# Performance work log

Hardware: AMD Instinct MI355X
Metric: run time of the kernel (lower is better)

## Reference

```python
import jax, jax.numpy as jnp
import numpy as np

BN_EPS = 1e-5  # torch BatchNorm1d default


def setup_inputs() -> dict:
    key = jax.random.key(0)
    k = jax.random.split(key, 5)
    B, D, L = 4096, 4096, 4  # batch, width, num layers (3 hidden + 1 output)
    x = jax.random.normal(k[0], (B, D), dtype=jnp.float32)
    # Per-layer Linear weights stored as [L, in, out]; scaled like xavier-ish init.
    W = jax.random.normal(k[1], (L, D, D), dtype=jnp.float32) * (1.0 / np.sqrt(D))
    b = jax.random.normal(k[2], (L, D), dtype=jnp.float32) * 0.01
    gamma = jax.random.uniform(k[3], (L, D), dtype=jnp.float32, minval=0.5, maxval=1.5)
    beta = jax.random.normal(k[4], (L, D), dtype=jnp.float32) * 0.1
    return {"x": x, "W": W, "b": b, "gamma": gamma, "beta": beta}


def _layer(h, W_l, b_l, gamma_l, beta_l):
    # one big GEMM replaces the per-neuron GEMV loop + stack
    h = h @ W_l + b_l  # [B, out]
    # BatchNorm1d, training mode: biased batch stats over the batch dim
    mu = jnp.mean(h, axis=0)
    var = jnp.var(h, axis=0)
    h = (h - mu) * jax.lax.rsqrt(var + BN_EPS) * gamma_l + beta_l
    return jax.nn.relu(h)


def reference(x, W, b, gamma, beta):
    out = x
    for l in range(W.shape[0]):  # small fixed layer count
        out = _layer(out, W[l], b[l], gamma[l], beta[l])
    # nn.Softmax(dim=0): softmax over the batch dimension, as in the original
    return jax.nn.softmax(out, axis=0)
```

## Files before the change

### kernel.cpp

```cpp
#include <hip/hip_runtime.h>
#include <stdint.h>

#define DIMD 4096
#define DIMB 4096
#define NLAYER 4
#define NT (DIMD / 64)

typedef unsigned short u16;
typedef __attribute__((ext_vector_type(4))) float f32x4;
typedef __attribute__((ext_vector_type(8))) __bf16 bf16x8;

__device__ __forceinline__ u16 f2bf(float f) {
    union { float f; uint32_t u; } v; v.f = f;
    return (u16)((v.u + 0x7fffu + ((v.u >> 16) & 1u)) >> 16);
}

__global__ void k_cvt(const float* __restrict__ in, u16* __restrict__ out) {
    int i = (blockIdx.x * 256 + threadIdx.x) * 4;
    float4 v = *reinterpret_cast<const float4*>(in + i);
    ushort4 r;
    r.x = f2bf(v.x); r.y = f2bf(v.y); r.z = f2bf(v.z); r.w = f2bf(v.w);
    *reinterpret_cast<ushort4*>(out + i) = r;
}

__global__ void k_trans(const float* __restrict__ W, u16* __restrict__ Wt) {
    __shared__ float tile[64][65];
    const int t = threadIdx.x;
    const int n0 = blockIdx.x * 64, k0 = blockIdx.y * 64;
    const int kr = t >> 4, c4 = (t & 15) * 4;
    #pragma unroll
    for (int r = 0; r < 4; ++r) {
        float4 v = *reinterpret_cast<const float4*>(W + (size_t)(k0 + kr + r * 16) * DIMD + n0 + c4);
        tile[kr + r * 16][c4 + 0] = v.x;
        tile[kr + r * 16][c4 + 1] = v.y;
        tile[kr + r * 16][c4 + 2] = v.z;
        tile[kr + r * 16][c4 + 3] = v.w;
    }
    __syncthreads();
    const int nr = t >> 4, k4 = (t & 15) * 4;
    #pragma unroll
    for (int r = 0; r < 4; ++r) {
        int n = nr + r * 16;
        ushort4 o;
        o.x = f2bf(tile[k4 + 0][n]);
        o.y = f2bf(tile[k4 + 1][n]);
        o.z = f2bf(tile[k4 + 2][n]);
        o.w = f2bf(tile[k4 + 3][n]);
        *reinterpret_cast<ushort4*>(Wt + (size_t)(n0 + n) * DIMD + k0 + k4) = o;
    }
}

#define GLD(g, l) __builtin_amdgcn_global_load_lds( \
    (__attribute__((address_space(1))) void*)(g),   \
    (__attribute__((address_space(3))) void*)(l), 16, 0, 0)

__global__ __launch_bounds__(512, 2) void k_gemm(
        const u16* __restrict__ A, const u16* __restrict__ Bt,
        const float* __restrict__ bias, float* __restrict__ C,
        float* __restrict__ csum, float* __restrict__ csum2) {
    __shared__ __attribute__((aligned(16))) u16 As[2 * 256 * 64];
    __shared__ __attribute__((aligned(16))) u16 Bs[2 * 256 * 64];
    const int tid = threadIdx.x;
    const int lane = tid & 63, wv = tid >> 6;
    const int wm = wv >> 2, wn = wv & 3;
    const int bm = blockIdx.y, bn = blockIdx.x;
    const int lr = lane & 15, lk = lane >> 4;

    const int r0 = tid >> 3;
    const int cswz = (tid & 7) ^ (r0 & 7);
    const u16* gA = A  + (size_t)(bm * 256 + r0) * DIMD + cswz * 8;
    const u16* gB = Bt + (size_t)(bn * 256 + r0) * DIMD + cswz * 8;

#define STAGE_A(h, t, buf) do { \
    const u16* _s = gA + (size_t)(h) * 128 * DIMD + (size_t)(t) * 64; \
    u16* _d = As + (buf) * 16384 + (h) * 8192 + wv * 512; \
    GLD(_s, _d); GLD(_s + (size_t)64 * DIMD, _d + 4096); \
} while (0)
#define STAGE_B(h, t, buf) do { \
    const u16* _s = gB + (size_t)(h) * 128 * DIMD + (size_t)(t) * 64; \
    u16* _d = Bs + (buf) * 16384 + (h) * 8192 + wv * 512; \
    GLD(_s, _d); GLD(_s + (size_t)64 * DIMD, _d + 4096); \
} while (0)

    int aoff[4][2], boff[2][2];
    #pragma unroll
    for (int mf = 0; mf < 4; ++mf)
        #pragma unroll
        for (int ks = 0; ks < 2; ++ks) {
            int row = wm * 128 + mf * 16 + lr;
            aoff[mf][ks] = row * 64 + ((ks * 4 + lk) ^ (row & 7)) * 8;
        }
    #pragma unroll
    for (int nf = 0; nf < 2; ++nf)
        #pragma unroll
        for (int ks = 0; ks < 2; ++ks) {
            int row = wn * 64 + nf * 16 + lr;
            boff[nf][ks] = row * 64 + ((ks * 4 + lk) ^ (row & 7)) * 8;
        }

    f32x4 acc[8][4] = {};
    bf16x8 a[4][2], b0[2][2], b1[2][2];

    STAGE_B(0, 0, 0); STAGE_B(1, 0, 0); STAGE_A(0, 0, 0); STAGE_A(1, 0, 0);
    STAGE_B(0, 1, 1); STAGE_B(1, 1, 1); STAGE_A(0, 1, 1); STAGE_A(1, 1, 1);
    asm volatile("s_waitcnt vmcnt(8)" ::: "memory");
    __builtin_amdgcn_s_barrier();

    for (int t = 0; t < NT; ++t) {
        const int cur = t & 1;
        const u16* Ab = As + cur * 16384;
        const u16* Bb = Bs + cur * 16384;
        const bool pf = (t + 2 < NT);

        #pragma unroll
        for (int mf = 0; mf < 4; ++mf)
            #pragma unroll
            for (int ks = 0; ks < 2; ++ks)
                a[mf][ks] = *reinterpret_cast<const bf16x8*>(Ab + aoff[mf][ks]);
        #pragma unroll
        for (int nf = 0; nf < 2; ++nf)
            #pragma unroll
            for (int ks = 0; ks < 2; ++ks)
                b0[nf][ks] = *reinterpret_cast<const bf16x8*>(Bb + boff[nf][ks]);
        __builtin_amdgcn_s_barrier();
        asm volatile("s_waitcnt lgkmcnt(0)" ::: "memory");
        __builtin_amdgcn_s_setprio(1);
        #pragma unroll
        for (int mf = 0; mf < 4; ++mf)
            #pragma unroll
            for (int nf = 0; nf < 2; ++nf)
                #pragma unroll
                for (int ks = 0; ks < 2; ++ks)
                    acc[mf][nf] = __builtin_amdgcn_mfma_f32_16x16x32_bf16(
                        a[mf][ks], b0[nf][ks], acc[mf][nf], 0, 0, 0);
        __builtin_amdgcn_s_setprio(0);
        __builtin_amdgcn_s_barrier();

        #pragma unroll
        for (int nf = 0; nf < 2; ++nf)
            #pragma unroll
            for (int ks = 0; ks < 2; ++ks)
                b1[nf][ks] = *reinterpret_cast<const bf16x8*>(Bb + 2048 + boff[nf][ks]);
        __builtin_amdgcn_s_barrier();
        asm volatile("s_waitcnt lgkmcnt(0)" ::: "memory");
        __builtin_amdgcn_s_setprio(1);
        #pragma unroll
        for (int mf = 0; mf < 4; ++mf)
            #pragma unroll
            for (int nf = 0; nf < 2; ++nf)
                #pragma unroll
                for (int ks = 0; ks < 2; ++ks)
                    acc[mf][2 + nf] = __builtin_amdgcn_mfma_f32_16x16x32_bf16(
                        a[mf][ks], b1[nf][ks], acc[mf][2 + nf], 0, 0, 0);
        __builtin_amdgcn_s_setprio(0);
        __builtin_amdgcn_s_barrier();

        #pragma unroll
        for (int mf = 0; mf < 4; ++mf)
            #pragma unroll
            for (int ks = 0; ks < 2; ++ks)
                a[mf][ks] = *reinterpret_cast<const bf16x8*>(Ab + 4096 + aoff[mf][ks]);
        if (pf) { STAGE_B(0, t + 2, cur); STAGE_B(1, t + 2, cur); }
        __builtin_amdgcn_s_barrier();
        asm volatile("s_waitcnt lgkmcnt(0)" ::: "memory");
        __builtin_amdgcn_s_setprio(1);
        #pragma unroll
        for (int mf = 0; mf < 4; ++mf)
            #pragma unroll
            for (int nf = 0; nf < 2; ++nf)
                #pragma unroll
                for (int ks = 0; ks < 2; ++ks)
                    acc[4 + mf][2 + nf] = __builtin_amdgcn_mfma_f32_16x16x32_bf16(
                        a[mf][ks], b1[nf][ks], acc[4 + mf][2 + nf], 0, 0, 0);
        __builtin_amdgcn_s_setprio(0);
        __builtin_amdgcn_s_barrier();

        if (pf) { STAGE_A(0, t + 2, cur); STAGE_A(1, t + 2, cur); }
        __builtin_amdgcn_s_setprio(1);
        #pragma unroll
        for (int mf = 0; mf < 4; ++mf)
            #pragma unroll
            for (int nf = 0; nf < 2; ++nf)
                #pragma unroll
                for (int ks = 0; ks < 2; ++ks)
                    acc[4 + mf][nf] = __builtin_amdgcn_mfma_f32_16x16x32_bf16(
                        a[mf][ks], b0[nf][ks], acc[4 + mf][nf], 0, 0, 0);
        __builtin_amdgcn_s_setprio(0);
        if (pf) asm volatile("s_waitcnt vmcnt(8)" ::: "memory");
        else    asm volatile("s_waitcnt vmcnt(0)" ::: "memory");
        __builtin_amdgcn_s_barrier();
    }

    #pragma unroll
    for (int nh = 0; nh < 2; ++nh)
        #pragma unroll
        for (int nf = 0; nf < 2; ++nf) {
            int n = nh * 2 + nf;
            int col = bn * 256 + wn * 64 + nh * 32 + nf * 16 + lr;
            float bv = bias[col];
            float s1 = 0.f, s2 = 0.f;
            #pragma unroll
            for (int m = 0; m < 8; ++m) {
                int rbase = bm * 256 + wm * 128 + (m >> 2) * 64 + (m & 3) * 16 + lk * 4;
                #pragma unroll
                for (int r = 0; r < 4; ++r) {
                    float v = acc[m][n][r] + bv;
                    C[(size_t)(rbase + r) * DIMD + col] = v;
                    s1 += v; s2 += v * v;
                }
            }
            s1 += __shfl_xor(s1, 16); s1 += __shfl_xor(s1, 32);
            s2 += __shfl_xor(s2, 16); s2 += __shfl_xor(s2, 32);
            if (lk == 0) {
                atomicAdd(&csum[col], s1);
                atomicAdd(&csum2[col], s2);
            }
        }
#undef STAGE_A
#undef STAGE_B
}

__global__ void k_bnfin(float* __restrict__ sum, float* __restrict__ sum2,
                        const float* __restrict__ gamma, const float* __restrict__ beta) {
    int j = blockIdx.x * 256 + threadIdx.x;
    float mu = sum[j] * (1.0f / DIMB);
    float var = sum2[j] * (1.0f / DIMB) - mu * mu;
    float rstd = rsqrtf(var + 1e-5f);
    float s = gamma[j] * rstd;
    sum[j] = s;
    sum2[j] = beta[j] - mu * s;
}

__global__ void k_norm(const float* __restrict__ H, const float* __restrict__ s,
                       const float* __restrict__ t, u16* __restrict__ o) {
    int j = blockIdx.x * 256 + threadIdx.x;
    int i0 = blockIdx.y * 128;
    float sj = s[j], tj = t[j];
    for (int i = i0; i < i0 + 128; ++i) {
        float v = fmaxf(H[(size_t)i * DIMD + j] * sj + tj, 0.0f);
        o[(size_t)i * DIMD + j] = f2bf(v);
    }
}

__global__ void k_normexp(float* __restrict__ H, const float* __restrict__ s,
                          const float* __restrict__ t, float* __restrict__ esum) {
    int j = blockIdx.x * 256 + threadIdx.x;
    int i0 = blockIdx.y * 128;
    float sj = s[j], tj = t[j];
    float acc = 0.f;
    for (int i = i0; i < i0 + 128; ++i) {
        float v = fmaxf(H[(size_t)i * DIMD + j] * sj + tj, 0.0f);
        float e = __expf(v);
        H[(size_t)i * DIMD + j] = e;
        acc += e;
    }
    atomicAdd(&esum[j], acc);
}

__global__ void k_div(float* __restrict__ H, const float* __restrict__ esum) {
    int i = (blockIdx.x * 256 + threadIdx.x) * 4;
    float4 v = *reinterpret_cast<const float4*>(H + i);
    const float4 e = *reinterpret_cast<const float4*>(esum + (i & (DIMD - 1)));
    v.x /= e.x; v.y /= e.y; v.z /= e.z; v.w /= e.w;
    *reinterpret_cast<float4*>(H + i) = v;
}

extern "C" void kernel_launch(void* const* d_in, const int* in_sizes, int n_in,
                              void* d_out, int out_size, void* d_ws, size_t ws_size,
                              hipStream_t stream) {
    (void)in_sizes; (void)n_in; (void)out_size; (void)ws_size;
    const float* x     = (const float*)d_in[0];
    const float* W     = (const float*)d_in[1];
    const float* b     = (const float*)d_in[2];
    const float* gamma = (const float*)d_in[3];
    const float* beta  = (const float*)d_in[4];
    float* out = (float*)d_out;

    char* ws = (char*)d_ws;
    u16*  Abf   = (u16*)ws;
    u16*  Wt    = (u16*)(ws + (size_t)32 * 1024 * 1024);
    float* stats = (float*)(ws + (size_t)64 * 1024 * 1024);
    hipMemsetAsync(stats, 0, (4 * 8192 + 4096) * sizeof(float), stream);

    k_cvt<<<DIMB * DIMD / 1024, 256, 0, stream>>>(x, Abf);

    for (int l = 0; l < NLAYER; ++l) {
        k_trans<<<dim3(64, 64), 256, 0, stream>>>(W + (size_t)l * DIMD * DIMD, Wt);
        float* sum = stats + l * 8192;
        float* sum2 = sum + 4096;
        k_gemm<<<dim3(16, 16), 512, 0, stream>>>(Abf, Wt, b + l * DIMD, out, sum, sum2);
        k_bnfin<<<16, 256, 0, stream>>>(sum, sum2, gamma + l * DIMD, beta + l * DIMD);
        if (l < NLAYER - 1)
            k_norm<<<dim3(16, 32), 256, 0, stream>>>(out, sum, sum2, Abf);
        else
            k_normexp<<<dim3(16, 32), 256, 0, stream>>>(out, sum, sum2, stats + 32768);
    }
    k_div<<<DIMB * DIMD / 1024, 256, 0, stream>>>(out, stats + 32768);
}
```

Before: 733.7 us.

## Restructure GEMM LDS schedule, batch weight transposes, fuse BN finalize into norm

The GEMM main loop now issues all LDS fragment reads earlier: the low-half A and both B halves are read up front and the high-half A is read between MFMA groups. This removes several intermediate barriers and issues all global prefetches together after a single barrier. All four weight transposes run in one 3D launch instead of one launch per layer, which needs more workspace. The BN finalize kernel is folded into the norm kernels, which are also widened to float4 per thread, cutting launches. The main risk is extra register pressure from the added A buffer and fewer barriers to hide LDS latency behind.

```diff
diff --git a/kernel.cpp b/kernel.cpp
--- a/kernel.cpp
+++ b/kernel.cpp
@@ -26,11 +26,12 @@
 __global__ void k_trans(const float* __restrict__ W, u16* __restrict__ Wt) {
     __shared__ float tile[64][65];
     const int t = threadIdx.x;
+    const size_t loff = (size_t)blockIdx.z * DIMD * DIMD;
     const int n0 = blockIdx.x * 64, k0 = blockIdx.y * 64;
     const int kr = t >> 4, c4 = (t & 15) * 4;
     #pragma unroll
     for (int r = 0; r < 4; ++r) {
-        float4 v = *reinterpret_cast<const float4*>(W + (size_t)(k0 + kr + r * 16) * DIMD + n0 + c4);
+        float4 v = *reinterpret_cast<const float4*>(W + loff + (size_t)(k0 + kr + r * 16) * DIMD + n0 + c4);
         tile[kr + r * 16][c4 + 0] = v.x;
         tile[kr + r * 16][c4 + 1] = v.y;
         tile[kr + r * 16][c4 + 2] = v.z;
@@ -46,7 +47,7 @@
         o.y = f2bf(tile[k4 + 1][n]);
         o.z = f2bf(tile[k4 + 2][n]);
         o.w = f2bf(tile[k4 + 3][n]);
-        *reinterpret_cast<ushort4*>(Wt + (size_t)(n0 + n) * DIMD + k0 + k4) = o;
+        *reinterpret_cast<ushort4*>(Wt + loff + (size_t)(n0 + n) * DIMD + k0 + k4) = o;
     }
 }
 
@@ -99,7 +100,7 @@
         }
 
     f32x4 acc[8][4] = {};
-    bf16x8 a[4][2], b0[2][2], b1[2][2];
+    bf16x8 al[4][2], ah[4][2], b0[2][2], b1[2][2];
 
     STAGE_B(0, 0, 0); STAGE_B(1, 0, 0); STAGE_A(0, 0, 0); STAGE_A(1, 0, 0);
     STAGE_B(0, 1, 1); STAGE_B(1, 1, 1); STAGE_A(0, 1, 1); STAGE_A(1, 1, 1);
@@ -116,14 +117,18 @@
         for (int mf = 0; mf < 4; ++mf)
             #pragma unroll
             for (int ks = 0; ks < 2; ++ks)
-                a[mf][ks] = *reinterpret_cast<const bf16x8*>(Ab + aoff[mf][ks]);
+                al[mf][ks] = *reinterpret_cast<const bf16x8*>(Ab + aoff[mf][ks]);
         #pragma unroll
         for (int nf = 0; nf < 2; ++nf)
             #pragma unroll
             for (int ks = 0; ks < 2; ++ks)
                 b0[nf][ks] = *reinterpret_cast<const bf16x8*>(Bb + boff[nf][ks]);
-        __builtin_amdgcn_s_barrier();
-        asm volatile("s_waitcnt lgkmcnt(0)" ::: "memory");
+        #pragma unroll
+        for (int nf = 0; nf < 2; ++nf)
+            #pragma unroll
+            for (int ks = 0; ks < 2; ++ks)
+                b1[nf][ks] = *reinterpret_cast<const bf16x8*>(Bb + 2048 + boff[nf][ks]);
+
         __builtin_amdgcn_s_setprio(1);
         #pragma unroll
         for (int mf = 0; mf < 4; ++mf)
@@ -132,17 +137,15 @@
                 #pragma unroll
                 for (int ks = 0; ks < 2; ++ks)
                     acc[mf][nf] = __builtin_amdgcn_mfma_f32_16x16x32_bf16(
-                        a[mf][ks], b0[nf][ks], acc[mf][nf], 0, 0, 0);
+                        al[mf][ks], b0[nf][ks], acc[mf][nf], 0, 0, 0);
         __builtin_amdgcn_s_setprio(0);
-        __builtin_amdgcn_s_barrier();
-
-        #pragma unroll
-        for (int nf = 0; nf < 2; ++nf)
+
+        #pragma unroll
+        for (int mf = 0; mf < 4; ++mf)
             #pragma unroll
             for (int ks = 0; ks < 2; ++ks)
-                b1[nf][ks] = *reinterpret_cast<const bf16x8*>(Bb + 2048 + boff[nf][ks]);
-        __builtin_amdgcn_s_barrier();
-        asm volatile("s_waitcnt lgkmcnt(0)" ::: "memory");
+                ah[mf][ks] = *reinterpret_cast<const bf16x8*>(Ab + 4096 + aoff[mf][ks]);
+
         __builtin_amdgcn_s_setprio(1);
         #pragma unroll
         for (int mf = 0; mf < 4; ++mf)
@@ -151,18 +154,18 @@
                 #pragma unroll
                 for (int ks = 0; ks < 2; ++ks)
                     acc[mf][2 + nf] = __builtin_amdgcn_mfma_f32_16x16x32_bf16(
-                        a[mf][ks], b1[nf][ks], acc[mf][2 + nf], 0, 0, 0);
+                        al[mf][ks], b1[nf][ks], acc[mf][2 + nf], 0, 0, 0);
         __builtin_amdgcn_s_setprio(0);
+
+        asm volatile("s_waitcnt lgkmcnt(0)" ::: "memory");
+        __builtin_amdgcn_sched_barrier(0);
         __builtin_amdgcn_s_barrier();
 
-        #pragma unroll
-        for (int mf = 0; mf < 4; ++mf)
-            #pragma unroll
-            for (int ks = 0; ks < 2; ++ks)
-                a[mf][ks] = *reinterpret_cast<const bf16x8*>(Ab + 4096 + aoff[mf][ks]);
-        if (pf) { STAGE_B(0, t + 2, cur); STAGE_B(1, t + 2, cur); }
-        __builtin_amdgcn_s_barrier();
-        asm volatile("s_waitcnt lgkmcnt(0)" ::: "memory");
+        if (pf) {
+            STAGE_B(0, t + 2, cur); STAGE_B(1, t + 2, cur);
+            STAGE_A(0, t + 2, cur); STAGE_A(1, t + 2, cur);
+        }
+
         __builtin_amdgcn_s_setprio(1);
         #pragma unroll
         for (int mf = 0; mf < 4; ++mf)
@@ -171,12 +174,7 @@
                 #pragma unroll
                 for (int ks = 0; ks < 2; ++ks)
                     acc[4 + mf][2 + nf] = __builtin_amdgcn_mfma_f32_16x16x32_bf16(
-                        a[mf][ks], b1[nf][ks], acc[4 + mf][2 + nf], 0, 0, 0);
-        __builtin_amdgcn_s_setprio(0);
-        __builtin_amdgcn_s_barrier();
-
-        if (pf) { STAGE_A(0, t + 2, cur); STAGE_A(1, t + 2, cur); }
-        __builtin_amdgcn_s_setprio(1);
+                        ah[mf][ks], b1[nf][ks], acc[4 + mf][2 + nf], 0, 0, 0);
         #pragma unroll
         for (int mf = 0; mf < 4; ++mf)
             #pragma unroll
@@ -184,8 +182,9 @@
                 #pragma unroll
                 for (int ks = 0; ks < 2; ++ks)
                     acc[4 + mf][nf] = __builtin_amdgcn_mfma_f32_16x16x32_bf16(
-                        a[mf][ks], b0[nf][ks], acc[4 + mf][nf], 0, 0, 0);
+                        ah[mf][ks], b0[nf][ks], acc[4 + mf][nf], 0, 0, 0);
         __builtin_amdgcn_s_setprio(0);
+
         if (pf) asm volatile("s_waitcnt vmcnt(8)" ::: "memory");
         else    asm volatile("s_waitcnt vmcnt(0)" ::: "memory");
         __builtin_amdgcn_s_barrier();
@@ -220,41 +219,62 @@
 #undef STAGE_B
 }
 
-__global__ void k_bnfin(float* __restrict__ sum, float* __restrict__ sum2,
-                        const float* __restrict__ gamma, const float* __restrict__ beta) {
-    int j = blockIdx.x * 256 + threadIdx.x;
-    float mu = sum[j] * (1.0f / DIMB);
-    float var = sum2[j] * (1.0f / DIMB) - mu * mu;
-    float rstd = rsqrtf(var + 1e-5f);
-    float s = gamma[j] * rstd;
-    sum[j] = s;
-    sum2[j] = beta[j] - mu * s;
-}
-
-__global__ void k_norm(const float* __restrict__ H, const float* __restrict__ s,
-                       const float* __restrict__ t, u16* __restrict__ o) {
-    int j = blockIdx.x * 256 + threadIdx.x;
+__global__ void k_norm(const float* __restrict__ H, const float* __restrict__ sum,
+                       const float* __restrict__ sum2, const float* __restrict__ gamma,
+                       const float* __restrict__ beta, u16* __restrict__ o) {
+    int j = (blockIdx.x * 256 + threadIdx.x) * 4;
     int i0 = blockIdx.y * 128;
-    float sj = s[j], tj = t[j];
+    float4 sm = *reinterpret_cast<const float4*>(sum + j);
+    float4 s2 = *reinterpret_cast<const float4*>(sum2 + j);
+    float4 gm = *reinterpret_cast<const float4*>(gamma + j);
+    float4 bt = *reinterpret_cast<const float4*>(beta + j);
+    float s[4], tt[4];
+    #pragma unroll
+    for (int c = 0; c < 4; ++c) {
+        float mu = (&sm.x)[c] * (1.0f / DIMB);
+        float var = (&s2.x)[c] * (1.0f / DIMB) - mu * mu;
+        s[c] = (&gm.x)[c] * rsqrtf(var + 1e-5f);
+        tt[c] = (&bt.x)[c] - mu * s[c];
+    }
     for (int i = i0; i < i0 + 128; ++i) {
-        float v = fmaxf(H[(size_t)i * DIMD + j] * sj + tj, 0.0f);
-        o[(size_t)i * DIMD + j] = f2bf(v);
-    }
-}
-
-__global__ void k_normexp(float* __restrict__ H, const float* __restrict__ s,
-                          const float* __restrict__ t, float* __restrict__ esum) {
-    int j = blockIdx.x * 256 + threadIdx.x;
+        float4 h = *reinterpret_cast<const float4*>(H + (size_t)i * DIMD + j);
+        ushort4 r;
+        #pragma unroll
+        for (int c = 0; c < 4; ++c)
+            (&r.x)[c] = f2bf(fmaxf((&h.x)[c] * s[c] + tt[c], 0.0f));
+        *reinterpret_cast<ushort4*>(o + (size_t)i * DIMD + j) = r;
+    }
+}
+
+__global__ void k_normexp(float* __restrict__ H, const float* __restrict__ sum,
+                          const float* __restrict__ sum2, const float* __restrict__ gamma,
+                          const float* __restrict__ beta, float* __restrict__ esum) {
+    int j = (blockIdx.x * 256 + threadIdx.x) * 4;
     int i0 = blockIdx.y * 128;
-    float sj = s[j], tj = t[j];
-    float acc = 0.f;
+    float4 sm = *reinterpret_cast<const float4*>(sum + j);
+    float4 s2 = *reinterpret_cast<const float4*>(sum2 + j);
+    float4 gm = *reinterpret_cast<const float4*>(gamma + j);
+    float4 bt = *reinterpret_cast<const float4*>(beta + j);
+    float s[4], tt[4], acc[4] = {0.f, 0.f, 0.f, 0.f};
+    #pragma unroll
+    for (int c = 0; c < 4; ++c) {
+        float mu = (&sm.x)[c] * (1.0f / DIMB);
+        float var = (&s2.x)[c] * (1.0f / DIMB) - mu * mu;
+        s[c] = (&gm.x)[c] * rsqrtf(var + 1e-5f);
+        tt[c] = (&bt.x)[c] - mu * s[c];
+    }
     for (int i = i0; i < i0 + 128; ++i) {
-        float v = fmaxf(H[(size_t)i * DIMD + j] * sj + tj, 0.0f);
-        float e = __expf(v);
-        H[(size_t)i * DIMD + j] = e;
-        acc += e;
-    }
-    atomicAdd(&esum[j], acc);
+        float4 h = *reinterpret_cast<const float4*>(H + (size_t)i * DIMD + j);
+        #pragma unroll
+        for (int c = 0; c < 4; ++c) {
+            float e = __expf(fmaxf((&h.x)[c] * s[c] + tt[c], 0.0f));
+            (&h.x)[c] = e;
+            acc[c] += e;
+        }
+        *reinterpret_cast<float4*>(H + (size_t)i * DIMD + j) = h;
+    }
+    #pragma unroll
+    for (int c = 0; c < 4; ++c) atomicAdd(&esum[j + c], acc[c]);
 }
 
 __global__ void k_div(float* __restrict__ H, const float* __restrict__ esum) {
@@ -277,23 +297,25 @@
     float* out = (float*)d_out;
 
     char* ws = (char*)d_ws;
-    u16*  Abf   = (u16*)ws;
-    u16*  Wt    = (u16*)(ws + (size_t)32 * 1024 * 1024);
-    float* stats = (float*)(ws + (size_t)64 * 1024 * 1024);
+    u16*  Abf = (u16*)ws;
+    u16*  Wt4 = (u16*)(ws + (size_t)32 * 1024 * 1024);
+    float* stats = (float*)(ws + (size_t)160 * 1024 * 1024);
     hipMemsetAsync(stats, 0, (4 * 8192 + 4096) * sizeof(float), stream);
 
     k_cvt<<<DIMB * DIMD / 1024, 256, 0, stream>>>(x, Abf);
+    k_trans<<<dim3(64, 64, 4), 256, 0, stream>>>(W, Wt4);
 
     for (int l = 0; l < NLAYER; ++l) {
-        k_trans<<<dim3(64, 64), 256, 0, stream>>>(W + (size_t)l * DIMD * DIMD, Wt);
         float* sum = stats + l * 8192;
         float* sum2 = sum + 4096;
-        k_gemm<<<dim3(16, 16), 512, 0, stream>>>(Abf, Wt, b + l * DIMD, out, sum, sum2);
-        k_bnfin<<<16, 256, 0, stream>>>(sum, sum2, gamma + l * DIMD, beta + l * DIMD);
+        k_gemm<<<dim3(16, 16), 512, 0, stream>>>(Abf, Wt4 + (size_t)l * DIMD * DIMD,
+                                                 b + l * DIMD, out, sum, sum2);
         if (l < NLAYER - 1)
-            k_norm<<<dim3(16, 32), 256, 0, stream>>>(out, sum, sum2, Abf);
+            k_norm<<<dim3(4, 32), 256, 0, stream>>>(out, sum, sum2,
+                gamma + l * DIMD, beta + l * DIMD, Abf);
         else
-            k_normexp<<<dim3(16, 32), 256, 0, stream>>>(out, sum, sum2, stats + 32768);
+            k_normexp<<<dim3(4, 32), 256, 0, stream>>>(out, sum, sum2,
+                gamma + l * DIMD, beta + l * DIMD, stats + 32768);
     }
     k_div<<<DIMB * DIMD / 1024, 256, 0, stream>>>(out, stats + 32768);
 }
```

New measurement: 793.4 us. 8.1% more time.
